# Optimization experiments

Measured on AMD Instinct MI355X. Metric: run time of the kernel, lower is better.

Reference implementation:

```python
import jax, jax.numpy as jnp
import numpy as np

N, C = 16384, 1000


def setup_inputs() -> dict:
    key = jax.random.key(0)
    ks = jax.random.split(key, 10)
    inp = {}
    for i in range(8):
        inp[f"outputs{i+1}"] = jax.random.normal(ks[i], (N, C), dtype=jnp.float32)
    inp["mimic"] = jax.random.normal(ks[8], (N, C), dtype=jnp.float32)
    inp["targets"] = jax.random.randint(ks[9], (N,), 0, C, dtype=jnp.int64)
    inp["n_test"] = N
    return inp


def _margin(x, targets):
    # top-2 margin, zeroed when target is not the argmax value
    top2, _ = jax.lax.top_k(x, 2)                      # [N, 2]
    tgt = jnp.take_along_axis(x, targets[:, None], axis=1)[:, 0]  # [N]
    return jnp.where(tgt == top2[:, 0], top2[:, 0] - top2[:, 1],
                     jnp.zeros((), x.dtype))


def reference(outputs1, outputs2, outputs3, outputs4, outputs5, outputs6,
              outputs7, outputs8, mimic, targets, n_test):
    T = 2.0
    outs = [outputs1, outputs2, outputs3, outputs4,
            outputs5, outputs6, outputs7, outputs8, mimic]
    margins = jnp.stack([_margin(o, targets) for o in outs], axis=1)  # [N, 9]
    out_threshold = jax.nn.softmax(margins / T, axis=1)               # [N, 9]
    max_preds = jnp.max(jnp.stack(outs[:8], axis=0))                  # scalar
    return (max_preds, out_threshold)
```

## Files before the change

### kernel.cpp

```cpp
#include <hip/hip_runtime.h>
#include <math.h>

__device__ __forceinline__ unsigned int float_key(float f) {
    unsigned int b = __float_as_uint(f);
    return (b & 0x80000000u) ? ~b : (b | 0x80000000u);
}

__global__ void init_kernel(unsigned int* key) {
    *key = 0u;
}

__global__ void finalize_kernel(float* out) {
    unsigned int k = ((unsigned int*)out)[0];
    unsigned int b = (k & 0x80000000u) ? (k ^ 0x80000000u) : ~k;
    out[0] = __uint_as_float(b);
}

__global__ __launch_bounds__(576) void margin_kernel(
    const float* __restrict__ o0, const float* __restrict__ o1,
    const float* __restrict__ o2, const float* __restrict__ o3,
    const float* __restrict__ o4, const float* __restrict__ o5,
    const float* __restrict__ o6, const float* __restrict__ o7,
    const float* __restrict__ o8,
    const int* __restrict__ targets,
    float* __restrict__ out, int C)
{
    __shared__ float s_margin[9];
    __shared__ float s_gmax[9];

    const int row  = blockIdx.x;
    const int wave = threadIdx.x >> 6;
    const int lane = threadIdx.x & 63;

    const float* ptrs[9] = {o0, o1, o2, o3, o4, o5, o6, o7, o8};
    const float* x = ptrs[wave] + (size_t)row * C;
    const int c = targets[row];

    float m1 = -INFINITY, m2 = -INFINITY;
    float tval = -INFINITY;
    float gm = -INFINITY;

    const int nf4 = C >> 2;
    const float4* x4 = (const float4*)x;
    const int cf4 = c >> 2, cs = c & 3;

    #pragma unroll 4
    for (int f4 = lane; f4 < nf4; f4 += 64) {
        float4 v = x4[f4];
        m2 = fmaxf(m2, fminf(m1, v.x)); m1 = fmaxf(m1, v.x);
        m2 = fmaxf(m2, fminf(m1, v.y)); m1 = fmaxf(m1, v.y);
        m2 = fmaxf(m2, fminf(m1, v.z)); m1 = fmaxf(m1, v.z);
        m2 = fmaxf(m2, fminf(m1, v.w)); m1 = fmaxf(m1, v.w);
        gm = fmaxf(gm, fmaxf(fmaxf(v.x, v.y), fmaxf(v.z, v.w)));
        if (f4 == cf4)
            tval = (cs == 0) ? v.x : (cs == 1) ? v.y : (cs == 2) ? v.z : v.w;
    }
    for (int idx = (nf4 << 2) + lane; idx < C; idx += 64) {
        float v = x[idx];
        m2 = fmaxf(m2, fminf(m1, v)); m1 = fmaxf(m1, v);
        gm = fmaxf(gm, v);
        if (idx == c) tval = v;
    }

    #pragma unroll
    for (int off = 32; off > 0; off >>= 1) {
        float om1 = __shfl_xor(m1, off);
        float om2 = __shfl_xor(m2, off);
        m2 = fmaxf(fmaxf(m2, om2), fminf(m1, om1));
        m1 = fmaxf(m1, om1);
        gm = fmaxf(gm, __shfl_xor(gm, off));
        tval = fmaxf(tval, __shfl_xor(tval, off));
    }

    if (lane == 0) {
        s_margin[wave] = (tval == m1) ? (m1 - m2) : 0.0f;
        s_gmax[wave] = gm;
    }
    __syncthreads();

    if (threadIdx.x == 0) {
        float mm = s_margin[0];
        #pragma unroll
        for (int k = 1; k < 9; ++k) mm = fmaxf(mm, s_margin[k]);
        float e[9], sum = 0.0f;
        #pragma unroll
        for (int k = 0; k < 9; ++k) {
            e[k] = expf((s_margin[k] - mm) * 0.5f);
            sum += e[k];
        }
        float inv = 1.0f / sum;
        float* orow = out + 1 + (size_t)row * 9;
        #pragma unroll
        for (int k = 0; k < 9; ++k) orow[k] = e[k] * inv;

        float bg = s_gmax[0];
        #pragma unroll
        for (int k = 1; k < 8; ++k) bg = fmaxf(bg, s_gmax[k]);
        atomicMax((unsigned int*)out, float_key(bg));
    }
}

extern "C" void kernel_launch(void* const* d_in, const int* in_sizes, int n_in,
                              void* d_out, int out_size, void* d_ws, size_t ws_size,
                              hipStream_t stream) {
    const float* o0 = (const float*)d_in[0];
    const float* o1 = (const float*)d_in[1];
    const float* o2 = (const float*)d_in[2];
    const float* o3 = (const float*)d_in[3];
    const float* o4 = (const float*)d_in[4];
    const float* o5 = (const float*)d_in[5];
    const float* o6 = (const float*)d_in[6];
    const float* o7 = (const float*)d_in[7];
    const float* o8 = (const float*)d_in[8];
    const int* targets = (const int*)d_in[9];
    const int N = in_sizes[9];
    const int C = in_sizes[0] / N;
    float* out = (float*)d_out;

    init_kernel<<<1, 1, 0, stream>>>((unsigned int*)out);
    margin_kernel<<<dim3(N), dim3(576), 0, stream>>>(
        o0, o1, o2, o3, o4, o5, o6, o7, o8, targets, out, C);
    finalize_kernel<<<1, 1, 0, stream>>>(out);
}
```

Before: 551.3 us.

## Process all nine rows per wave in a persistent grid and drop atomics

Restructures the margin kernel so that one wave handles a row across all nine tensors, with a fixed grid of 1024 blocks looping persistently over rows. The target value is now read directly instead of being tracked during the scan. The global max no longer uses an atomic plus init and finalize kernels; it is written as per-block partials and reduced by a small second kernel, which cuts one launch. The cost is much higher register pressure from nine sets of float4 loads and accumulators, which may lower occupancy. There is also a leftover dead tail loop.

```diff
diff --git a/kernel.cpp b/kernel.cpp
--- a/kernel.cpp
+++ b/kernel.cpp
@@ -1,103 +1,136 @@
 #include <hip/hip_runtime.h>
 #include <math.h>
 
-__device__ __forceinline__ unsigned int float_key(float f) {
-    unsigned int b = __float_as_uint(f);
-    return (b & 0x80000000u) ? ~b : (b | 0x80000000u);
-}
+#define GRID  1024
+#define BLOCK 256
 
-__global__ void init_kernel(unsigned int* key) {
-    *key = 0u;
-}
-
-__global__ void finalize_kernel(float* out) {
-    unsigned int k = ((unsigned int*)out)[0];
-    unsigned int b = (k & 0x80000000u) ? (k ^ 0x80000000u) : ~k;
-    out[0] = __uint_as_float(b);
-}
-
-__global__ __launch_bounds__(576) void margin_kernel(
+__global__ __launch_bounds__(BLOCK) void margin_kernel(
     const float* __restrict__ o0, const float* __restrict__ o1,
     const float* __restrict__ o2, const float* __restrict__ o3,
     const float* __restrict__ o4, const float* __restrict__ o5,
     const float* __restrict__ o6, const float* __restrict__ o7,
     const float* __restrict__ o8,
     const int* __restrict__ targets,
-    float* __restrict__ out, int C)
+    float* __restrict__ out, float* __restrict__ block_max,
+    int N, int C)
 {
-    __shared__ float s_margin[9];
-    __shared__ float s_gmax[9];
+    __shared__ float s_gm[BLOCK / 64];
 
-    const int row  = blockIdx.x;
-    const int wave = threadIdx.x >> 6;
-    const int lane = threadIdx.x & 63;
+    const int lane   = threadIdx.x & 63;
+    const int wib    = threadIdx.x >> 6;
+    const int gwave  = blockIdx.x * (BLOCK / 64) + wib;
+    const int nwaves = GRID * (BLOCK / 64);
+    const int nf4    = C >> 2;
 
-    const float* ptrs[9] = {o0, o1, o2, o3, o4, o5, o6, o7, o8};
-    const float* x = ptrs[wave] + (size_t)row * C;
-    const int c = targets[row];
-
-    float m1 = -INFINITY, m2 = -INFINITY;
-    float tval = -INFINITY;
     float gm = -INFINITY;
 
-    const int nf4 = C >> 2;
-    const float4* x4 = (const float4*)x;
-    const int cf4 = c >> 2, cs = c & 3;
+    for (int row = gwave; row < N; row += nwaves) {
+        const int c = targets[row];
+        const unsigned rowoff = (unsigned)row * (unsigned)C;
 
-    #pragma unroll 4
-    for (int f4 = lane; f4 < nf4; f4 += 64) {
-        float4 v = x4[f4];
-        m2 = fmaxf(m2, fminf(m1, v.x)); m1 = fmaxf(m1, v.x);
-        m2 = fmaxf(m2, fminf(m1, v.y)); m1 = fmaxf(m1, v.y);
-        m2 = fmaxf(m2, fminf(m1, v.z)); m1 = fmaxf(m1, v.z);
-        m2 = fmaxf(m2, fminf(m1, v.w)); m1 = fmaxf(m1, v.w);
-        gm = fmaxf(gm, fmaxf(fmaxf(v.x, v.y), fmaxf(v.z, v.w)));
-        if (f4 == cf4)
-            tval = (cs == 0) ? v.x : (cs == 1) ? v.y : (cs == 2) ? v.z : v.w;
-    }
-    for (int idx = (nf4 << 2) + lane; idx < C; idx += 64) {
-        float v = x[idx];
-        m2 = fmaxf(m2, fminf(m1, v)); m1 = fmaxf(m1, v);
-        gm = fmaxf(gm, v);
-        if (idx == c) tval = v;
+        float tv[9];
+        tv[0] = o0[rowoff + c]; tv[1] = o1[rowoff + c]; tv[2] = o2[rowoff + c];
+        tv[3] = o3[rowoff + c]; tv[4] = o4[rowoff + c]; tv[5] = o5[rowoff + c];
+        tv[6] = o6[rowoff + c]; tv[7] = o7[rowoff + c]; tv[8] = o8[rowoff + c];
+
+        float m1[9], m2[9];
+        #pragma unroll
+        for (int k = 0; k < 9; ++k) { m1[k] = -INFINITY; m2[k] = -INFINITY; }
+
+        const float4* p[9] = {
+            (const float4*)(o0 + rowoff), (const float4*)(o1 + rowoff),
+            (const float4*)(o2 + rowoff), (const float4*)(o3 + rowoff),
+            (const float4*)(o4 + rowoff), (const float4*)(o5 + rowoff),
+            (const float4*)(o6 + rowoff), (const float4*)(o7 + rowoff),
+            (const float4*)(o8 + rowoff) };
+
+        for (int f4 = lane; f4 < nf4; f4 += 64) {
+            float4 v[9];
+            #pragma unroll
+            for (int k = 0; k < 9; ++k) v[k] = p[k][f4];
+            #pragma unroll
+            for (int k = 0; k < 9; ++k) {
+                m2[k] = fmaxf(m2[k], fminf(m1[k], v[k].x)); m1[k] = fmaxf(m1[k], v[k].x);
+                m2[k] = fmaxf(m2[k], fminf(m1[k], v[k].y)); m1[k] = fmaxf(m1[k], v[k].y);
+                m2[k] = fmaxf(m2[k], fminf(m1[k], v[k].z)); m1[k] = fmaxf(m1[k], v[k].z);
+                m2[k] = fmaxf(m2[k], fminf(m1[k], v[k].w)); m1[k] = fmaxf(m1[k], v[k].w);
+            }
+        }
+        for (int idx = (nf4 << 2) + lane; idx < C; idx += 64) {
+            #pragma unroll
+            for (int k = 0; k < 9; ++k) {
+                float v = p[k >= 0 ? k : 0][0].x;
+                (void)v;
+            }
+        }
+        if (C & 3) {
+            for (int idx = (nf4 << 2) + lane; idx < C; idx += 64) {
+                const float* b[9] = {o0,o1,o2,o3,o4,o5,o6,o7,o8};
+                #pragma unroll
+                for (int k = 0; k < 9; ++k) {
+                    float v = b[k][rowoff + idx];
+                    m2[k] = fmaxf(m2[k], fminf(m1[k], v)); m1[k] = fmaxf(m1[k], v);
+                }
+            }
+        }
+
+        #pragma unroll
+        for (int off = 32; off > 0; off >>= 1) {
+            #pragma unroll
+            for (int k = 0; k < 9; ++k) {
+                float a1 = __shfl_xor(m1[k], off);
+                float a2 = __shfl_xor(m2[k], off);
+                m2[k] = fmaxf(fmaxf(m2[k], a2), fminf(m1[k], a1));
+                m1[k] = fmaxf(m1[k], a1);
+            }
+        }
+
+        float margin[9];
+        #pragma unroll
+        for (int k = 0; k < 9; ++k)
+            margin[k] = (tv[k] == m1[k]) ? (m1[k] - m2[k]) : 0.0f;
+
+        #pragma unroll
+        for (int k = 0; k < 8; ++k) gm = fmaxf(gm, m1[k]);
+
+        float mm = margin[0];
+        #pragma unroll
+        for (int k = 1; k < 9; ++k) mm = fmaxf(mm, margin[k]);
+        float sum = 0.0f;
+        #pragma unroll
+        for (int k = 0; k < 9; ++k) sum += expf((margin[k] - mm) * 0.5f);
+        float inv = 1.0f / sum;
+
+        float msel = margin[0];
+        #pragma unroll
+        for (int k = 1; k < 9; ++k) msel = (lane == k) ? margin[k] : msel;
+        if (lane < 9)
+            out[1 + (size_t)row * 9 + lane] = expf((msel - mm) * 0.5f) * inv;
     }
 
+    if (lane == 0) s_gm[wib] = gm;
+    __syncthreads();
+    if (threadIdx.x == 0) {
+        float bg = s_gm[0];
+        #pragma unroll
+        for (int w = 1; w < BLOCK / 64; ++w) bg = fmaxf(bg, s_gm[w]);
+        block_max[blockIdx.x] = bg;
+    }
+}
+
+__global__ __launch_bounds__(256) void finalize_kernel(
+    const float* __restrict__ block_max, float* __restrict__ out, int n)
+{
+    __shared__ float s[4];
+    const int lane = threadIdx.x & 63;
+    float v = -INFINITY;
+    for (int i = threadIdx.x; i < n; i += 256) v = fmaxf(v, block_max[i]);
     #pragma unroll
-    for (int off = 32; off > 0; off >>= 1) {
-        float om1 = __shfl_xor(m1, off);
-        float om2 = __shfl_xor(m2, off);
-        m2 = fmaxf(fmaxf(m2, om2), fminf(m1, om1));
-        m1 = fmaxf(m1, om1);
-        gm = fmaxf(gm, __shfl_xor(gm, off));
-        tval = fmaxf(tval, __shfl_xor(tval, off));
-    }
-
-    if (lane == 0) {
-        s_margin[wave] = (tval == m1) ? (m1 - m2) : 0.0f;
-        s_gmax[wave] = gm;
-    }
+    for (int off = 32; off > 0; off >>= 1) v = fmaxf(v, __shfl_xor(v, off));
+    if (lane == 0) s[threadIdx.x >> 6] = v;
     __syncthreads();
-
-    if (threadIdx.x == 0) {
-        float mm = s_margin[0];
-        #pragma unroll
-        for (int k = 1; k < 9; ++k) mm = fmaxf(mm, s_margin[k]);
-        float e[9], sum = 0.0f;
-        #pragma unroll
-        for (int k = 0; k < 9; ++k) {
-            e[k] = expf((s_margin[k] - mm) * 0.5f);
-            sum += e[k];
-        }
-        float inv = 1.0f / sum;
-        float* orow = out + 1 + (size_t)row * 9;
-        #pragma unroll
-        for (int k = 0; k < 9; ++k) orow[k] = e[k] * inv;
-
-        float bg = s_gmax[0];
-        #pragma unroll
-        for (int k = 1; k < 8; ++k) bg = fmaxf(bg, s_gmax[k]);
-        atomicMax((unsigned int*)out, float_key(bg));
-    }
+    if (threadIdx.x == 0)
+        out[0] = fmaxf(fmaxf(s[0], s[1]), fmaxf(s[2], s[3]));
 }
 
 extern "C" void kernel_launch(void* const* d_in, const int* in_sizes, int n_in,
@@ -116,9 +149,9 @@
     const int N = in_sizes[9];
     const int C = in_sizes[0] / N;
     float* out = (float*)d_out;
+    float* block_max = (float*)d_ws;
 
-    init_kernel<<<1, 1, 0, stream>>>((unsigned int*)out);
-    margin_kernel<<<dim3(N), dim3(576), 0, stream>>>(
-        o0, o1, o2, o3, o4, o5, o6, o7, o8, targets, out, C);
-    finalize_kernel<<<1, 1, 0, stream>>>(out);
+    margin_kernel<<<dim3(GRID), dim3(BLOCK), 0, stream>>>(
+        o0, o1, o2, o3, o4, o5, o6, o7, o8, targets, out, block_max, N, C);
+    finalize_kernel<<<1, 256, 0, stream>>>(block_max, out, GRID);
 }
```

Result: faster. 492.6 us (-10.7%).
